# Performance work log

Measured on AMD Instinct MI355X. Metric: run time of the kernel, lower is better.

## Reference

```python
import jax, jax.numpy as jnp
import numpy as np

B, N, NE = 2, 100000, 800000
S, F, D = 3, 2, 128          # space_size, n_fields, enc_dim
TD, CD, SD = 11, 32, 10      # enc_t_dim, cond_dim, spatial_dim


def _mlp(x, w1, b1, w2, b2):
    # Linear -> SiLU -> Linear (MLP with n_hidden=1, hidden=128, no layernorm)
    return jax.nn.silu(x @ w1 + b1) @ w2 + b2


def setup_inputs() -> dict:
    key = jax.random.key(0)
    ks = iter(jax.random.split(key, 40))

    def w(shape):
        fan_in = shape[-2] if len(shape) >= 2 else shape[-1]
        return jax.random.normal(next(ks), shape, jnp.float32) / np.sqrt(fan_in)

    def b(shape):
        return jnp.zeros(shape, jnp.float32)

    inp = dict(
        node_pos=jax.random.normal(next(ks), (B, N, S), jnp.float32),
        state_in=jax.random.normal(next(ks), (B, N, F), jnp.float32),
        time_i=jax.random.normal(next(ks), (B, TD), jnp.float32),
        conditions=jax.random.normal(next(ks), (B, CD), jnp.float32),
        spatial_inform=jax.random.normal(next(ks), (B, SD), jnp.float32),
        edges=jax.random.randint(next(ks), (B, NE, 2), 0, N, jnp.int64)
        if jax.config.jax_enable_x64 else jax.random.randint(next(ks), (B, NE, 2), 0, N, jnp.int32),
        # per-field node MLPs, stacked over fields: input = space_size + 1
        fields_w1=w((F, S + 1, D)), fields_b1=b((F, D)),
        fields_w2=w((F, D, D)), fields_b2=b((F, D)),
        # time / cond / spatial MLPs
        time_w1=w((TD, D)), time_b1=b((D,)), time_w2=w((D, D)), time_b2=b((D,)),
        cond_w1=w((CD, D)), cond_b1=b((D,)), cond_w2=w((D, D)), cond_b2=b((D,)),
        spat_w1=w((SD, D)), spat_b1=b((D,)), spat_w2=w((D, D)), spat_b2=b((D,)),
        # fuse_para: 3*D -> 128 -> 2*D
        fuse_w1=w((3 * D, D)), fuse_b1=b((D,)),
        fuse_w2=w((D, 2 * D)), fuse_b2=b((2 * D,)),
        # edge MLP: 2*S+1 -> 128 -> D
        fe_w1=w((2 * S + 1, D)), fe_b1=b((D,)),
        fe_w2=w((D, D)), fe_b2=b((D,)),
    )
    return inp


def reference(node_pos, state_in, time_i, conditions, spatial_inform, edges,
              fields_w1, fields_b1, fields_w2, fields_b2,
              time_w1, time_b1, time_w2, time_b2,
              cond_w1, cond_b1, cond_w2, cond_b2,
              spat_w1, spat_b1, spat_w2, spat_b2,
              fuse_w1, fuse_b1, fuse_w2, fuse_b2,
              fe_w1, fe_b1, fe_w2, fe_b2):
    # FiLM parameters from time + condition + spatial encodings
    time_enc = _mlp(time_i, time_w1, time_b1, time_w2, time_b2)        # [B,D]
    cond_enc = _mlp(conditions, cond_w1, cond_b1, cond_w2, cond_b2)    # [B,D]
    spat_enc = _mlp(spatial_inform, spat_w1, spat_b1, spat_w2, spat_b2)
    h = jnp.concatenate([cond_enc, time_enc, spat_enc], axis=-1)       # [B,3D]
    para = _mlp(h, fuse_w1, fuse_b1, fuse_w2, fuse_b2)                 # [B,2D]
    gamma, beta = jnp.split(para, 2, axis=-1)                          # [B,D] each

    # Per-field node MLPs, vectorized over fields: x_f [B,N,F,S+1]
    pos_b = jnp.broadcast_to(node_pos[:, :, None, :], (node_pos.shape[0], node_pos.shape[1], F, S))
    x_f = jnp.concatenate([pos_b, state_in[..., None]], axis=-1)       # [B,N,F,S+1]
    hid = jax.nn.silu(jnp.einsum('bnfd,fde->bnfe', x_f, fields_w1) + fields_b1)
    V = jnp.einsum('bnfe,feo->bnfo', hid, fields_w2) + fields_b2       # [B,N,F,D]
    V = V * gamma[:, None, None, :] + beta[:, None, None, :]

    # Edge features: gather sender/receiver positions, diff/norm/concat
    idx_s = jnp.broadcast_to(edges[..., 0:1], edges.shape[:2] + (S,))
    idx_r = jnp.broadcast_to(edges[..., 1:2], edges.shape[:2] + (S,))
    senders = jnp.take_along_axis(node_pos, idx_s, axis=1)             # [B,NE,S]
    receivers = jnp.take_along_axis(node_pos, idx_r, axis=1)
    d = receivers - senders
    norm = jnp.sqrt(jnp.sum(d * d, axis=-1, keepdims=True) + 1e-8)
    e_feat = jnp.concatenate([d, -d, norm], axis=-1)                   # [B,NE,2S+1]
    E = _mlp(e_feat, fe_w1, fe_b1, fe_w2, fe_b2)                       # [B,NE,D]

    return V, E
```

## Files before the change

### kernel.cpp

```cpp
#include <hip/hip_runtime.h>
#include <hip/hip_bf16.h>
#include <string.h>

#define B_  2
#define N_  100000
#define NE_ 800000
#define F_  2
#define D_  128
#define TD_ 11
#define CD_ 32
#define SD_ 10

#define NODE_BX   782
#define NODE_NB   (NODE_BX * F_ * B_)
#define EDGE_BX   6250
#define EDGE_NB   (EDGE_BX * B_)
#define GROUPS    3125
#define TOTAL_NB  (NODE_NB + EDGE_NB)

#define WS_GB      0
#define WS_FLAG    2048
#define WS_W1FRAG  2112
#define WS_W2FRAG  26688

typedef short s16x8 __attribute__((ext_vector_type(8)));
typedef float f32x4 __attribute__((ext_vector_type(4)));
typedef unsigned u32x4 __attribute__((ext_vector_type(4)));

static __device__ __forceinline__ unsigned short f2bf(float f) {
    unsigned u = __builtin_bit_cast(unsigned, f);
    u += 0x7FFFu + ((u >> 16) & 1u);
    return (unsigned short)(u >> 16);
}
static __device__ __forceinline__ float silu_f(float x) {
    return x * __builtin_amdgcn_rcpf(1.0f + __expf(-x));
}
static __device__ __forceinline__ unsigned pack_bf16(float lo, float hi) {
    __hip_bfloat162 c = __float22bfloat162_rn(make_float2(lo, hi));
    unsigned r;
    memcpy(&r, &c, sizeof(r));
    return r;
}
static __device__ __forceinline__ void lds_barrier() {
    asm volatile("s_waitcnt lgkmcnt(0)" ::: "memory");
    __builtin_amdgcn_s_barrier();
}

__global__ void prep_kernel(
    const float* __restrict__ time_i, const float* __restrict__ cond,
    const float* __restrict__ spat,
    const float* tw1, const float* tb1, const float* tw2, const float* tb2,
    const float* cw1, const float* cb1, const float* cw2, const float* cb2,
    const float* sw1, const float* sb1, const float* sw2, const float* sb2,
    const float* fuw1, const float* fub1, const float* fuw2, const float* fub2,
    const float* __restrict__ fw1, const float* __restrict__ fb1,
    const float* __restrict__ fw2,
    const float* __restrict__ ew1, const float* __restrict__ eb1,
    const float* __restrict__ ew2,
    const int* __restrict__ edges,
    char* __restrict__ ws)
{
    const int bx = blockIdx.x, t = threadIdx.x;

    if (bx < 2) {
        const int b = bx, d = t;
        __shared__ float h[3 * D_];
        __shared__ float hid[D_];

        const float* X [3] = { cond + b * CD_, time_i + b * TD_, spat + b * SD_ };
        const float* W1[3] = { cw1, tw1, sw1 };
        const float* B1[3] = { cb1, tb1, sb1 };
        const float* W2[3] = { cw2, tw2, sw2 };
        const float* B2[3] = { cb2, tb2, sb2 };
        const int    K [3] = { CD_, TD_, SD_ };

        for (int m = 0; m < 3; ++m) {
            float a = 0.f;
            if (d < D_) {
                a = B1[m][d];
                for (int k = 0; k < K[m]; ++k) a += X[m][k] * W1[m][k * D_ + d];
            }
            __syncthreads();
            if (d < D_) hid[d] = a / (1.0f + __expf(-a));
            __syncthreads();
            if (d < D_) {
                float o = B2[m][d];
                for (int k = 0; k < D_; ++k) o += hid[k] * W2[m][k * D_ + d];
                h[m * D_ + d] = o;
            }
        }
        __syncthreads();
        float pre2 = 0.f;
        if (d < D_) {
            pre2 = fub1[d];
            for (int k = 0; k < 3 * D_; ++k) pre2 += h[k] * fuw1[k * D_ + d];
        }
        __syncthreads();
        if (d < D_) hid[d] = pre2 / (1.0f + __expf(-pre2));
        __syncthreads();
        if (d < D_) {
            float g = fub2[d], be = fub2[D_ + d];
            for (int k = 0; k < D_; ++k) {
                float hv = hid[k];
                g  += hv * fuw2[k * 2 * D_ + d];
                be += hv * fuw2[k * 2 * D_ + D_ + d];
            }
            float* gb = (float*)ws;
            gb[(b * 2 + 0) * D_ + d] = g;
            gb[(b * 2 + 1) * D_ + d] = be;
        }
    } else if (bx < 5) {
        const int which = bx - 2;
        const float* src = (which < 2) ? (fw2 + which * D_ * D_) : ew2;
        unsigned short* dst = (unsigned short*)(ws + WS_W2FRAG) + (long)which * 2048 * 8;
        for (int e = t; e < 2048; e += 256) {
            const int lanee = e & 63, kb = (e >> 6) & 3, nt = e >> 8;
            const int out = nt * 16 + (lanee & 15);
            const int k0  = kb * 32 + (lanee >> 4) * 8;
            s16x8 v;
            #pragma unroll
            for (int i = 0; i < 8; ++i)
                v[i] = (short)f2bf(src[(k0 + i) * D_ + out]);
            *(s16x8*)(dst + e * 8) = v;
        }
    } else {
        if (t == 0) {
            int nz = 0;
            for (int j = 0; j < 64; ++j) nz |= edges[2 * j + 1];
            ((float*)(ws + WS_FLAG))[0] = (nz == 0) ? 1.0f : 0.0f;
        }
        unsigned short* w1f = (unsigned short*)(ws + WS_W1FRAG);
        for (int e = t; e < 1536; e += 256) {
            const int which = e >> 9;
            const int h8    = (e >> 6) & 7;
            const int lane  = e & 63;
            const int m  = h8 * 16 + (lane & 15);
            const int kg = lane >> 4;
            s16x8 v;
            #pragma unroll
            for (int i = 0; i < 8; ++i) {
                const int k = kg * 8 + i;
                float val = 0.f;
                if (kg == 0) {
                    if (which < 2) {
                        if (k < 4)      val = fw1[(which * 4 + k) * D_ + m];
                        else if (k == 4) val = fb1[which * D_ + m];
                    } else {
                        if (k < 3)      val = ew1[k * D_ + m] - ew1[(k + 3) * D_ + m];
                        else if (k == 3) val = ew1[6 * D_ + m];
                        else if (k == 4) val = eb1[m];
                    }
                }
                v[i] = (short)f2bf(val);
            }
            *(s16x8*)(w1f + e * 8) = v;
        }
    }
}

__global__ __launch_bounds__(256, 3) void fused_kernel(
    const float* __restrict__ pos, const float* __restrict__ state,
    const int* __restrict__ edges,
    const float* __restrict__ fb2, const float* __restrict__ eb2,
    const char* __restrict__ ws,
    float* __restrict__ V, float* __restrict__ E)
{
    __shared__ __align__(16) char smem[50176];
    unsigned short* w2lds = (unsigned short*)smem;
    float* outF = (float*)smem;

    const int bx = blockIdx.x, t = threadIdx.x;
    const int lane = t & 63, wv = t >> 6;
    const int kg = lane >> 4, lr = lane & 15;

    const float* gbAll = (const float*)ws;
    const char*  w1fB  = ws + WS_W1FRAG;
    const unsigned short* w2all = (const unsigned short*)(ws + WS_W2FRAG);

    bool isNode; int sub;
    if (bx >= 5 * GROUPS) { isNode = true; sub = GROUPS + (bx - 5 * GROUPS); }
    else {
        int g = bx / 5, s = bx - 5 * g;
        if (s == 0) { isNode = true;  sub = g; }
        else        { isNode = false; sub = g * 4 + (s - 1); }
    }

    float xa[4], xb[4];
    int n0 = 0, f = 0, b, e0blk = 0;
    if (isNode) {
        n0 = (sub % NODE_BX) * 128;
        f  = (sub / NODE_BX) & 1;
        b  = sub / (NODE_BX * F_);
        int na = n0 + wv * 32 + lr;      if (na >= N_) na = N_ - 1;
        int nb = n0 + wv * 32 + lr + 16; if (nb >= N_) nb = N_ - 1;
        long pa = ((long)b * N_ + na) * 3, pb = ((long)b * N_ + nb) * 3;
        xa[0] = pos[pa]; xa[1] = pos[pa + 1]; xa[2] = pos[pa + 2];
        xb[0] = pos[pb]; xb[1] = pos[pb + 1]; xb[2] = pos[pb + 2];
        xa[3] = state[((long)b * N_ + na) * F_ + f];
        xb[3] = state[((long)b * N_ + nb) * F_ + f];
    } else {
        e0blk = (sub % EDGE_BX) * 128;
        b     = sub / EDGE_BX;
        const bool x64 = ((const float*)(ws + WS_FLAG))[0] > 0.5f;
        const long ea = (long)b * NE_ + e0blk + wv * 32 + lr;
        const long eb = ea + 16;
        int sa, ra, sb, rb;
        if (x64) {
            sa = edges[ea * 4]; ra = edges[ea * 4 + 2];
            sb = edges[eb * 4]; rb = edges[eb * 4 + 2];
        } else {
            int2 va = *(const int2*)(edges + ea * 2); sa = va.x; ra = va.y;
            int2 vb = *(const int2*)(edges + eb * 2); sb = vb.x; rb = vb.y;
        }
        const float* pp = pos + (long)b * N_ * 3;
        {
            long so = (long)sa * 3, ro = (long)ra * 3;
            xa[0] = pp[ro]     - pp[so];
            xa[1] = pp[ro + 1] - pp[so + 1];
            xa[2] = pp[ro + 2] - pp[so + 2];
            xa[3] = sqrtf(xa[0]*xa[0] + xa[1]*xa[1] + xa[2]*xa[2] + 1e-8f);
        }
        {
            long so = (long)sb * 3, ro = (long)rb * 3;
            xb[0] = pp[ro]     - pp[so];
            xb[1] = pp[ro + 1] - pp[so + 1];
            xb[2] = pp[ro + 2] - pp[so + 2];
            xb[3] = sqrtf(xb[0]*xb[0] + xb[1]*xb[1] + xb[2]*xb[2] + 1e-8f);
        }
    }

    const int which = isNode ? f : 2;

    {
        const char* src = (const char*)(w2all + (long)which * 2048 * 8);
        #pragma unroll
        for (int j = 0; j < 8; ++j) {
            f32x4 v = *(const f32x4*)(src + (j * 256 + t) * 16);
            *(f32x4*)((char*)w2lds + (j * 256 + t) * 16) = v;
        }
    }
    __syncthreads();

    u32x4 bf0, bf1;
    bf0[0] = pack_bf16(xa[0], xa[1]); bf0[1] = pack_bf16(xa[2], xa[3]);
    bf0[2] = 0x00003F80u;             bf0[3] = 0u;
    bf1[0] = pack_bf16(xb[0], xb[1]); bf1[1] = pack_bf16(xb[2], xb[3]);
    bf1[2] = 0x00003F80u;             bf1[3] = 0u;

    char* slabB = smem + 32768 + wv * 4352;
    const char* w1fr = w1fB + which * 8192;

    f32x4 acc[2][8];
    #pragma unroll
    for (int rt = 0; rt < 2; ++rt)
        #pragma unroll
        for (int nt = 0; nt < 8; ++nt) acc[rt][nt] = (f32x4){0.f, 0.f, 0.f, 0.f};

    const f32x4 zero4 = (f32x4){0.f, 0.f, 0.f, 0.f};

    #pragma unroll
    for (int rt = 0; rt < 2; ++rt) {
        s16x8 bop;
        { u32x4 tmp = rt ? bf1 : bf0; memcpy(&bop, &tmp, sizeof(bop)); }

        #pragma unroll
        for (int h8 = 0; h8 < 8; ++h8) {
            s16x8 af = *(const s16x8*)(w1fr + h8 * 1024 + lane * 16);
            f32x4 h4 = __builtin_amdgcn_mfma_f32_16x16x32_bf16(af, bop, zero4, 0, 0, 0);
            uint2 d;
            d.x = pack_bf16(silu_f(h4[0]), silu_f(h4[1]));
            d.y = pack_bf16(silu_f(h4[2]), silu_f(h4[3]));
            *(uint2*)(slabB + lr * 272 + h8 * 32 + kg * 8) = d;
        }
        lds_barrier();

        #pragma unroll
        for (int kb = 0; kb < 4; ++kb) {
            s16x8 u = *(const s16x8*)(slabB + lr * 272 + kb * 64 + kg * 16);
            #pragma unroll
            for (int nt = 0; nt < 8; ++nt) {
                s16x8 afr = *(const s16x8*)(w2lds + ((nt * 4 + kb) * 64 + lane) * 8);
                acc[rt][nt] = __builtin_amdgcn_mfma_f32_16x16x32_bf16(afr, u, acc[rt][nt], 0, 0, 0);
            }
        }
        lds_barrier();
    }

    const float* bias  = isNode ? (fb2 + f * D_) : eb2;
    const float* gamma = gbAll + b * 2 * D_;
    const float* beta  = gamma + D_;
    float* base = isNode ? (V + (((long)b * N_ + n0) * F_ + f) * D_)
                         : (E + ((long)b * NE_ + e0blk) * D_);
    const long stride   = isNode ? (long)F_ * D_ : (long)D_;
    const int rowsValid = isNode ? (N_ - n0) : 128;

    #pragma unroll
    for (int p = 0; p < 2; ++p) {
        #pragma unroll
        for (int ntl = 0; ntl < 4; ++ntl) {
            const int nt = p * 4 + ntl;
            const int d0 = nt * 16 + kg * 4;
            const f32x4 bs = *(const f32x4*)(bias + d0);
            f32x4 g, be;
            if (isNode) { g = *(const f32x4*)(gamma + d0); be = *(const f32x4*)(beta + d0); }
            #pragma unroll
            for (int mt = 0; mt < 2; ++mt) {
                const int m = wv * 32 + mt * 16 + lr;
                f32x4 v;
                #pragma unroll
                for (int r = 0; r < 4; ++r)
                    v[r] = isNode ? (acc[mt][nt][r] + bs[r]) * g[r] + be[r]
                                  : acc[mt][nt][r] + bs[r];
                *(f32x4*)(outF + m * 68 + ntl * 16 + kg * 4) = v;
            }
        }
        lds_barrier();
        #pragma unroll
        for (int j = 0; j < 8; ++j) {
            const int r = wv * 32 + j * 4 + (lane >> 4);
            const int c = (lane & 15) * 4;
            f32x4 v = *(const f32x4*)(outF + r * 68 + c);
            if (r < rowsValid)
                __builtin_nontemporal_store(v, (f32x4*)(base + (long)r * stride + p * 64 + c));
        }
        if (p == 0) lds_barrier();
    }
}

extern "C" void kernel_launch(void* const* d_in, const int* in_sizes, int n_in,
                              void* d_out, int out_size, void* d_ws, size_t ws_size,
                              hipStream_t stream)
{
    (void)in_sizes; (void)n_in; (void)out_size; (void)ws_size;

    const float* node_pos  = (const float*)d_in[0];
    const float* state_in  = (const float*)d_in[1];
    const float* time_i    = (const float*)d_in[2];
    const float* conditions= (const float*)d_in[3];
    const float* spatial   = (const float*)d_in[4];
    const int*   edges     = (const int*)d_in[5];
    const float* fields_w1 = (const float*)d_in[6];
    const float* fields_b1 = (const float*)d_in[7];
    const float* fields_w2 = (const float*)d_in[8];
    const float* fields_b2 = (const float*)d_in[9];
    const float* tw1 = (const float*)d_in[10];
    const float* tb1 = (const float*)d_in[11];
    const float* tw2 = (const float*)d_in[12];
    const float* tb2 = (const float*)d_in[13];
    const float* cw1 = (const float*)d_in[14];
    const float* cb1 = (const float*)d_in[15];
    const float* cw2 = (const float*)d_in[16];
    const float* cb2 = (const float*)d_in[17];
    const float* sw1 = (const float*)d_in[18];
    const float* sb1 = (const float*)d_in[19];
    const float* sw2 = (const float*)d_in[20];
    const float* sb2 = (const float*)d_in[21];
    const float* fu_w1 = (const float*)d_in[22];
    const float* fu_b1 = (const float*)d_in[23];
    const float* fu_w2 = (const float*)d_in[24];
    const float* fu_b2 = (const float*)d_in[25];
    const float* fe_w1 = (const float*)d_in[26];
    const float* fe_b1 = (const float*)d_in[27];
    const float* fe_w2 = (const float*)d_in[28];
    const float* fe_b2 = (const float*)d_in[29];

    char*  ws = (char*)d_ws;
    float* V  = (float*)d_out;
    float* E  = V + (long)B_ * N_ * F_ * D_;

    prep_kernel<<<dim3(6), dim3(256), 0, stream>>>(
        time_i, conditions, spatial,
        tw1, tb1, tw2, tb2, cw1, cb1, cw2, cb2, sw1, sb1, sw2, sb2,
        fu_w1, fu_b1, fu_w2, fu_b2,
        fields_w1, fields_b1, fields_w2,
        fe_w1, fe_b1, fe_w2,
        edges, ws);

    fused_kernel<<<dim3(TOTAL_NB), dim3(256), 0, stream>>>(
        node_pos, state_in, edges, fields_b2, fe_b2, ws, V, E);
}
```

Measured before the change: 245.8 us.

## Keep SiLU hidden activations in registers by permuting W2 fragment K order

The W2 fragment layout is permuted along the K dimension so that the first-layer MFMA output fragments can feed the second-layer MFMA B operand directly from registers. This removes the per-wave LDS slab round trip and its barriers. Shared memory per block drops, so launch bounds are raised to four blocks per CU for more occupancy. In exchange the kernel holds more live registers, which could cause spills under the tighter occupancy bound.

```diff
diff --git a/kernel.cpp b/kernel.cpp
--- a/kernel.cpp
+++ b/kernel.cpp
@@ -116,11 +116,14 @@
         for (int e = t; e < 2048; e += 256) {
             const int lanee = e & 63, kb = (e >> 6) & 3, nt = e >> 8;
             const int out = nt * 16 + (lanee & 15);
-            const int k0  = kb * 32 + (lanee >> 4) * 8;
+            const int kgA = lanee >> 4;
             s16x8 v;
             #pragma unroll
-            for (int i = 0; i < 8; ++i)
-                v[i] = (short)f2bf(src[(k0 + i) * D_ + out]);
+            for (int i = 0; i < 8; ++i) {
+                const int hid = kb * 32 + ((i >> 2) << 4) + kgA * 4
+                              + (((i >> 1) & 1) << 1) + (i & 1);
+                v[i] = (short)f2bf(src[hid * D_ + out]);
+            }
             *(s16x8*)(dst + e * 8) = v;
         }
     } else {
@@ -158,14 +161,14 @@
     }
 }
 
-__global__ __launch_bounds__(256, 3) void fused_kernel(
+__global__ __launch_bounds__(256, 4) void fused_kernel(
     const float* __restrict__ pos, const float* __restrict__ state,
     const int* __restrict__ edges,
     const float* __restrict__ fb2, const float* __restrict__ eb2,
     const char* __restrict__ ws,
     float* __restrict__ V, float* __restrict__ E)
 {
-    __shared__ __align__(16) char smem[50176];
+    __shared__ __align__(16) char smem[34816];
     unsigned short* w2lds = (unsigned short*)smem;
     float* outF = (float*)smem;
 
@@ -241,13 +244,6 @@
     }
     __syncthreads();
 
-    u32x4 bf0, bf1;
-    bf0[0] = pack_bf16(xa[0], xa[1]); bf0[1] = pack_bf16(xa[2], xa[3]);
-    bf0[2] = 0x00003F80u;             bf0[3] = 0u;
-    bf1[0] = pack_bf16(xb[0], xb[1]); bf1[1] = pack_bf16(xb[2], xb[3]);
-    bf1[2] = 0x00003F80u;             bf1[3] = 0u;
-
-    char* slabB = smem + 32768 + wv * 4352;
     const char* w1fr = w1fB + which * 8192;
 
     f32x4 acc[2][8];
@@ -261,29 +257,38 @@
     #pragma unroll
     for (int rt = 0; rt < 2; ++rt) {
         s16x8 bop;
-        { u32x4 tmp = rt ? bf1 : bf0; memcpy(&bop, &tmp, sizeof(bop)); }
-
+        {
+            u32x4 bf;
+            const float* x = rt ? xb : xa;
+            bf[0] = pack_bf16(x[0], x[1]);
+            bf[1] = pack_bf16(x[2], x[3]);
+            bf[2] = 0x00003F80u;
+            bf[3] = 0u;
+            memcpy(&bop, &bf, sizeof(bop));
+        }
+
+        uint2 d[8];
         #pragma unroll
         for (int h8 = 0; h8 < 8; ++h8) {
             s16x8 af = *(const s16x8*)(w1fr + h8 * 1024 + lane * 16);
             f32x4 h4 = __builtin_amdgcn_mfma_f32_16x16x32_bf16(af, bop, zero4, 0, 0, 0);
-            uint2 d;
-            d.x = pack_bf16(silu_f(h4[0]), silu_f(h4[1]));
-            d.y = pack_bf16(silu_f(h4[2]), silu_f(h4[3]));
-            *(uint2*)(slabB + lr * 272 + h8 * 32 + kg * 8) = d;
-        }
-        lds_barrier();
+            d[h8].x = pack_bf16(silu_f(h4[0]), silu_f(h4[1]));
+            d[h8].y = pack_bf16(silu_f(h4[2]), silu_f(h4[3]));
+        }
 
         #pragma unroll
         for (int kb = 0; kb < 4; ++kb) {
-            s16x8 u = *(const s16x8*)(slabB + lr * 272 + kb * 64 + kg * 16);
+            u32x4 uw;
+            uw[0] = d[2 * kb].x;     uw[1] = d[2 * kb].y;
+            uw[2] = d[2 * kb + 1].x; uw[3] = d[2 * kb + 1].y;
+            s16x8 u;
+            memcpy(&u, &uw, sizeof(u));
             #pragma unroll
             for (int nt = 0; nt < 8; ++nt) {
                 s16x8 afr = *(const s16x8*)(w2lds + ((nt * 4 + kb) * 64 + lane) * 8);
                 acc[rt][nt] = __builtin_amdgcn_mfma_f32_16x16x32_bf16(afr, u, acc[rt][nt], 0, 0, 0);
             }
         }
-        lds_barrier();
     }
 
     const float* bias  = isNode ? (fb2 + f * D_) : eb2;
@@ -293,6 +298,8 @@
                          : (E + ((long)b * NE_ + e0blk) * D_);
     const long stride   = isNode ? (long)F_ * D_ : (long)D_;
     const int rowsValid = isNode ? (N_ - n0) : 128;
+
+    lds_barrier();
 
     #pragma unroll
     for (int p = 0; p < 2; ++p) {
```

Measured after the change: 474.8 us. +93.1%, slower.
